# Kernel tuning notes

Measured on AMD Instinct MI355X. Metric: run time of the kernel, lower is better.

The kernel has to match this reference:

```python
import jax, jax.numpy as jnp
import numpy as np

# dims: batch, nodes, d_node, d_edge, d_attn_hid, heads, d_node_hid, d_edge_hid, layers
B, N, DN, DE, DH, H, DNH, DEH, L = 2, 256, 128, 64, 128, 8, 512, 256, 2
DHH = DH // H  # per-head dim
SCALE = 1.0 / (DH ** 0.5)  # source scales by full d_hid, not per-head dim


def _ln(x, g, b):
    m = jnp.mean(x, -1, keepdims=True)
    v = jnp.mean((x - m) ** 2, -1, keepdims=True)
    return (x - m) * jax.lax.rsqrt(v + 1e-5) * g + b


def _gelu(x):
    return jax.nn.gelu(x, approximate=False)  # torch nn.GELU default = exact erf


def setup_inputs() -> dict:
    key = jax.random.key(0)
    ks = iter(jax.random.split(key, 40))
    def w(shape, scale=0.02):
        return jax.random.normal(next(ks), shape, jnp.float32) * scale
    return {
        "node_features": jax.random.normal(next(ks), (B, N, DN), jnp.float32),
        "edge_features": jax.random.normal(next(ks), (B, N, N, DE), jnp.float32),
        "Wqkv_n": w((L, DN, 3 * DH)),
        "Wqkv_e": w((L, DE, 4 * DH)),
        "Wo": w((L, DH, DN)), "bo": jnp.zeros((L, DN), jnp.float32),
        "Wl0": w((L, DN, DN)), "bl0": jnp.zeros((L, DN), jnp.float32),
        "ln0_g": jnp.ones((L, DN), jnp.float32), "ln0_b": jnp.zeros((L, DN), jnp.float32),
        "Wm1": w((L, DN, DNH)), "Wm2": w((L, DNH, DN)), "bm2": jnp.zeros((L, DN), jnp.float32),
        "ln1_g": jnp.ones((L, DN), jnp.float32), "ln1_b": jnp.zeros((L, DN), jnp.float32),
        "We0": w((L, 2 * DE, DEH)), "be0": jnp.zeros((L, DEH), jnp.float32),
        "Ws": w((L, DN, DEH)), "bs": jnp.zeros((L, DEH), jnp.float32),
        "Wt": w((L, DN, DEH)), "bt": jnp.zeros((L, DEH), jnp.float32),
        "We1": w((L, DEH, DE)), "be1": jnp.zeros((L, DE), jnp.float32),
        "eln0_g": jnp.ones((L, DE), jnp.float32), "eln0_b": jnp.zeros((L, DE), jnp.float32),
        "Wem1": w((L, DE, DEH)), "Wem2": w((L, DEH, DE)), "bem2": jnp.zeros((L, DE), jnp.float32),
        "eln1_g": jnp.ones((L, DE), jnp.float32), "eln1_b": jnp.zeros((L, DE), jnp.float32),
    }


def _forward(node_features, edge_features, Wqkv_n, Wqkv_e, Wo, bo, Wl0, bl0,
             ln0_g, ln0_b, Wm1, Wm2, bm2, ln1_g, ln1_b, We0, be0, Ws, bs, Wt, bt,
             We1, be1, eln0_g, eln0_b, Wem1, Wem2, bem2, eln1_g, eln1_b):
    x, e = node_features, edge_features
    for l in range(L):
        # --- RTAttention (modulate_v=True, eval mode) ---
        qkv_n = (x @ Wqkv_n[l]).reshape(B, N, H, 3 * DHH).transpose(0, 2, 1, 3)  # b h n 3d
        qn, kn, vn = jnp.split(qkv_n, 3, axis=-1)
        qkv_e = (e @ Wqkv_e[l]).reshape(B, N, N, H, 4 * DHH).transpose(0, 3, 1, 2, 4)  # b h i j 4d
        eq, ek, ev, em = jnp.split(qkv_e, 4, axis=-1)
        q = qn[:, :, :, None, :] + eq            # b h i j d
        k = kn[:, :, None, :, :] + ek            # b h i j d
        v = vn[:, :, None, :, :] * em + ev       # modulated values
        dots = SCALE * jnp.einsum('bhijd,bhijd->bhij', q, k)
        attn = jax.nn.softmax(dots, axis=-1)
        out = jnp.einsum('bhij,bhijd->bhid', attn, v)
        out = out.transpose(0, 2, 1, 3).reshape(B, N, DH)
        attn_out = out @ Wo[l] + bo[l]
        # --- node updates: ln(x + lin0(attn)); ln(x + mlp(x)) ---
        x = _ln(x + (attn_out @ Wl0[l] + bl0[l]), ln0_g[l], ln0_b[l])
        x = _ln(x + (_gelu(x @ Wm1[l]) @ Wm2[l] + bm2[l]), ln1_g[l], ln1_b[l])
        # --- edge updates (EdgeLayer) ---
        src = (x @ Ws[l] + bs[l])[:, :, None, :]   # broadcast over target j
        tgt = (x @ Wt[l] + bt[l])[:, None, :, :]   # broadcast over source i
        ecat = jnp.concatenate([e, e.transpose(0, 2, 1, 3)], axis=-1)  # [e_ij, e_ji]
        h = _gelu(ecat @ We0[l] + be0[l] + src + tgt)
        e = _ln(e + (h @ We1[l] + be1[l]), eln0_g[l], eln0_b[l])
        e = _ln(e + (_gelu(e @ Wem1[l]) @ Wem2[l] + bem2[l]), eln1_g[l], eln1_b[l])
    return x, e


def reference(node_features, edge_features, Wqkv_n, Wqkv_e, Wo, bo, Wl0, bl0,
              ln0_g, ln0_b, Wm1, Wm2, bm2, ln1_g, ln1_b, We0, be0, Ws, bs, Wt, bt,
              We1, be1, eln0_g, eln0_b, Wem1, Wem2, bem2, eln1_g, eln1_b):
    return _forward(node_features, edge_features, Wqkv_n, Wqkv_e, Wo, bo, Wl0, bl0,
                    ln0_g, ln0_b, Wm1, Wm2, bm2, ln1_g, ln1_b, We0, be0, Ws, bs, Wt, bt,
                    We1, be1, eln0_g, eln0_b, Wem1, Wem2, bem2, eln1_g, eln1_b)
```

## Files before the change

### kernel.cpp

```cpp
#include <hip/hip_runtime.h>
#include <hip/hip_bf16.h>
#include <stdint.h>

#define BB 2
#define NN 256
#define DN 128
#define DE 64
#define DH 128
#define NH 8
#define DHH 16
#define DNH 512
#define DEH 256
#define NL 2
#define SCALE_ATT 0.08838834764831845f

typedef __hip_bfloat16 bf16;
typedef __attribute__((ext_vector_type(8))) short short8;
typedef __attribute__((ext_vector_type(4))) float f32x4;

__device__ __forceinline__ float gelu_f(float x) {
  return 0.5f * x * (1.0f + erff(x * 0.70710678118654752f));
}
__device__ __forceinline__ float gelu_t(float x) {
  float m2u = x * fmaf(x * x, -0.07135481627f, -1.59576912161f);
  float e = __expf(m2u);
  return x * __builtin_amdgcn_rcpf(1.f + e);
}

__device__ __forceinline__ float wave_sum(float v) {
#pragma unroll
  for (int o = 32; o > 0; o >>= 1) v += __shfl_xor(v, o, 64);
  return v;
}

__device__ __forceinline__ short f2bf(float f) {
  union { float f; uint32_t u; } v{f};
  uint32_t r = (v.u + 0x7FFFu + ((v.u >> 16) & 1u)) >> 16;
  return (short)r;
}
__device__ __forceinline__ float bf2f(short s) {
  union { uint32_t u; float f; } v;
  v.u = ((uint32_t)(uint16_t)s) << 16;
  return v.f;
}

__global__ void k_detect(const uint32_t* g8, const uint32_t* g13, int* flag) {
  if (threadIdx.x == 0 && blockIdx.x == 0) {
    uint32_t a = g8[0], b = g13[0];
    *flag = (a == 0x3F803F80u || b == 0x3F803F80u) ? 1 : 0;
  }
}

struct CastArgs {
  const void* src[30];
  float* dst[30];
  int n[30];
  const int* flag;
};

__global__ __launch_bounds__(256) void k_cast_all(CastArgs a) {
  int ti = blockIdx.y;
  float* d = a.dst[ti];
  int n = a.n[ti];
  int stride = gridDim.x * blockDim.x;
  if (*a.flag) {
    const bf16* s = (const bf16*)a.src[ti];
    for (int i = blockIdx.x * blockDim.x + threadIdx.x; i < n; i += stride)
      d[i] = __bfloat162float(s[i]);
  } else {
    const float* s = (const float*)a.src[ti];
    for (int i = blockIdx.x * blockDim.x + threadIdx.x; i < n; i += stride)
      d[i] = s[i];
  }
}

__global__ __launch_bounds__(256) void k_cast_e(const void* __restrict__ src,
                                                short* __restrict__ dst,
                                                const int* __restrict__ flag) {
  const int n8 = BB * NN * NN * DE / 8;
  int stride = gridDim.x * blockDim.x;
  if (*flag) {
    const uint4* s = (const uint4*)src;
    uint4* d = (uint4*)dst;
    for (int i = blockIdx.x * blockDim.x + threadIdx.x; i < n8; i += stride) d[i] = s[i];
  } else {
    const float4* s = (const float4*)src;
    for (int i = blockIdx.x * blockDim.x + threadIdx.x; i < n8; i += stride) {
      float4 a = s[2 * i], b = s[2 * i + 1];
      short* o = dst + 8 * i;
      o[0] = f2bf(a.x); o[1] = f2bf(a.y); o[2] = f2bf(a.z); o[3] = f2bf(a.w);
      o[4] = f2bf(b.x); o[5] = f2bf(b.y); o[6] = f2bf(b.z); o[7] = f2bf(b.w);
    }
  }
}

__global__ __launch_bounds__(256) void k_cast_out(const float* __restrict__ x,
                                                  const short* __restrict__ e,
                                                  void* __restrict__ out_v,
                                                  const int* __restrict__ flag) {
  const int nx = BB * NN * DN;
  const int total = nx + BB * NN * NN * DE;
  int stride = gridDim.x * blockDim.x;
  if (*flag) {
    short* out = (short*)out_v;
    for (int i = blockIdx.x * blockDim.x + threadIdx.x; i < total; i += stride)
      out[i] = (i < nx) ? f2bf(x[i]) : e[i - nx];
  } else {
    float* out = (float*)out_v;
    for (int i = blockIdx.x * blockDim.x + threadIdx.x; i < total; i += stride)
      out[i] = (i < nx) ? x[i] : bf2f(e[i - nx]);
  }
}

struct WtJob { const float* src; short* dst; int K; int N; };
struct WtArgs { WtJob job[10]; };
__global__ __launch_bounds__(256) void k_wtrans_all(WtArgs a) {
  WtJob j = a.job[blockIdx.y];
  int total = j.K * j.N;
  int stride = gridDim.x * 256;
  for (int idx = blockIdx.x * 256 + threadIdx.x; idx < total; idx += stride) {
    int k = idx / j.N, n = idx - k * j.N;
    j.dst[n * j.K + k] = f2bf(j.src[idx]);
  }
}

__global__ __launch_bounds__(128) void k_node_qkv(const float* __restrict__ x,
                                                  const float* __restrict__ W,
                                                  float* __restrict__ qkv) {
  int row = blockIdx.x;
  __shared__ float xs[DN];
  int t = threadIdx.x;
  xs[t] = x[row * DN + t];
  __syncthreads();
#pragma unroll
  for (int c0 = 0; c0 < 384; c0 += 128) {
    int c = c0 + t;
    float a = 0.f;
    for (int k = 0; k < DN; ++k) a = fmaf(xs[k], W[k * 384 + c], a);
    qkv[row * 384 + c] = a;
  }
}

__global__ __launch_bounds__(256) void k_attn_fused(
    const short* __restrict__ e, const short* __restrict__ WqeT,
    const float* __restrict__ qkv, float* __restrict__ o_buf) {
  int i = blockIdx.x, b = blockIdx.y;
  __shared__ short est[256 * 72];
  __shared__ float sp[NH * NN];
  __shared__ float qnl[DH];
  int t = threadIdx.x;
  for (int idx = t; idx < 2048; idx += 256) {
    int j = idx >> 3, c8 = (idx & 7) * 8;
    *(short8*)(est + j * 72 + c8) =
        *(const short8*)(e + ((size_t)(b * NN + i) * NN + j) * DE + c8);
  }
  if (t < DH) qnl[t] = qkv[(size_t)(b * NN + i) * 384 + (t >> 4) * 48 + (t & 15)];
  __syncthreads();

  int wv = t >> 6, lane = t & 63, g8 = lane >> 4, lo = lane & 15;

  {
    short8 bq[2][2][2];
#pragma unroll
    for (int hh = 0; hh < 2; ++hh)
#pragma unroll
      for (int p = 0; p < 2; ++p)
#pragma unroll
        for (int ks = 0; ks < 2; ++ks)
          bq[hh][p][ks] = *(const short8*)(
              WqeT + (size_t)(((wv * 2 + hh) * 4 + p) * 16 + lo) * 64 + ks * 32 + g8 * 8);
    for (int mt = 0; mt < 16; ++mt) {
      short8 a0 = *(const short8*)(est + (mt * 16 + lo) * 72 + g8 * 8);
      short8 a1 = *(const short8*)(est + (mt * 16 + lo) * 72 + 32 + g8 * 8);
#pragma unroll
      for (int hh = 0; hh < 2; ++hh) {
        int h = wv * 2 + hh;
        float kn4[4];
#pragma unroll
        for (int r = 0; r < 4; ++r)
          kn4[r] = qkv[(size_t)(b * NN + mt * 16 + g8 * 4 + r) * 384 + h * 48 + 16 + lo];
        f32x4 cq = {0.f, 0.f, 0.f, 0.f}, ck = {0.f, 0.f, 0.f, 0.f};
        cq = __builtin_amdgcn_mfma_f32_16x16x32_bf16(a0, bq[hh][0][0], cq, 0, 0, 0);
        cq = __builtin_amdgcn_mfma_f32_16x16x32_bf16(a1, bq[hh][0][1], cq, 0, 0, 0);
        ck = __builtin_amdgcn_mfma_f32_16x16x32_bf16(a0, bq[hh][1][0], ck, 0, 0, 0);
        ck = __builtin_amdgcn_mfma_f32_16x16x32_bf16(a1, bq[hh][1][1], ck, 0, 0, 0);
        float qv = qnl[h * 16 + lo];
#pragma unroll
        for (int r = 0; r < 4; ++r) {
          int j = mt * 16 + g8 * 4 + r;
          float s = (qv + cq[r]) * (kn4[r] + ck[r]);
#pragma unroll
          for (int off = 1; off < 16; off <<= 1) s += __shfl_xor(s, off, 64);
          if (lo == 0) sp[h * NN + j] = s * SCALE_ATT;
        }
      }
    }
  }
  __syncthreads();

#pragma unroll
  for (int hh = 0; hh < 2; ++hh) {
    int h = wv * 2 + hh;
    float v[4];
#pragma unroll
    for (int q = 0; q < 4; ++q) v[q] = sp[h * NN + lane + 64 * q];
    float m = fmaxf(fmaxf(v[0], v[1]), fmaxf(v[2], v[3]));
#pragma unroll
    for (int o = 32; o > 0; o >>= 1) m = fmaxf(m, __shfl_xor(m, o, 64));
    float l = 0.f;
#pragma unroll
    for (int q = 0; q < 4; ++q) { v[q] = __expf(v[q] - m); l += v[q]; }
    l = wave_sum(l);
    float inv = 1.f / l;
#pragma unroll
    for (int q = 0; q < 4; ++q) sp[h * NN + lane + 64 * q] = v[q] * inv;
  }
  __syncthreads();

  {
    short8 bv[2][2][2];
#pragma unroll
    for (int hh = 0; hh < 2; ++hh)
#pragma unroll
      for (int p = 0; p < 2; ++p)
#pragma unroll
        for (int ks = 0; ks < 2; ++ks)
          bv[hh][p][ks] = *(const short8*)(
              WqeT + (size_t)(((wv * 2 + hh) * 4 + 2 + p) * 16 + lo) * 64 + ks * 32 + g8 * 8);
    float oacc[2] = {0.f, 0.f};
    for (int mt = 0; mt < 16; ++mt) {
      short8 a0 = *(const short8*)(est + (mt * 16 + lo) * 72 + g8 * 8);
      short8 a1 = *(const short8*)(est + (mt * 16 + lo) * 72 + 32 + g8 * 8);
#pragma unroll
      for (int hh = 0; hh < 2; ++hh) {
        int h = wv * 2 + hh;
        float vn4[4];
#pragma unroll
        for (int r = 0; r < 4; ++r)
          vn4[r] = qkv[(size_t)(b * NN + mt * 16 + g8 * 4 + r) * 384 + h * 48 + 32 + lo];
        f32x4 cv = {0.f, 0.f, 0.f, 0.f}, cm = {0.f, 0.f, 0.f, 0.f};
        cv = __builtin_amdgcn_mfma_f32_16x16x32_bf16(a0, bv[hh][0][0], cv, 0, 0, 0);
        cv = __builtin_amdgcn_mfma_f32_16x16x32_bf16(a1, bv[hh][0][1], cv, 0, 0, 0);
        cm = __builtin_amdgcn_mfma_f32_16x16x32_bf16(a0, bv[hh][1][0], cm, 0, 0, 0);
        cm = __builtin_amdgcn_mfma_f32_16x16x32_bf16(a1, bv[hh][1][1], cm, 0, 0, 0);
#pragma unroll
        for (int r = 0; r < 4; ++r) {
          int j = mt * 16 + g8 * 4 + r;
          float vv = fmaf(vn4[r], cm[r], cv[r]);
          oacc[hh] = fmaf(sp[h * NN + j], vv, oacc[hh]);
        }
      }
    }
#pragma unroll
    for (int hh = 0; hh < 2; ++hh) {
      int h = wv * 2 + hh;
      float o = oacc[hh];
      o += __shfl_xor(o, 16, 64);
      o += __shfl_xor(o, 32, 64);
      if (g8 == 0) o_buf[(size_t)(b * NN + i) * DH + h * 16 + lo] = o;
    }
  }
}

__global__ __launch_bounds__(128) void k_node_fused(
    const float* __restrict__ o_buf,
    const float* __restrict__ Wo, const float* __restrict__ bo,
    const float* __restrict__ Wl0, const float* __restrict__ bl0,
    const float* __restrict__ g0, const float* __restrict__ b0n,
    const float* __restrict__ Wm1, const float* __restrict__ Wm2,
    const float* __restrict__ bm2, const float* __restrict__ g1,
    const float* __restrict__ b1n, const float* __restrict__ Ws,
    const float* __restrict__ bs, const float* __restrict__ Wt,
    const float* __restrict__ bt, const float* __restrict__ WqnN,
    float* __restrict__ qkv, float* __restrict__ srcb,
    float* __restrict__ tgtb, float* __restrict__ x) {
  int i = blockIdx.x, b = blockIdx.y;
  int row = b * NN + i;
  __shared__ float orow[DH];
  __shared__ float t1[DH];
  __shared__ float xs[DN];
  __shared__ float hs[DNH];
  __shared__ float red[4];
  int t = threadIdx.x;
  orow[t] = o_buf[(size_t)row * DH + t];
  __syncthreads();
  {
    float a = bo[t];
    for (int k = 0; k < DH; ++k) a = fmaf(orow[k], Wo[k * DN + t], a);
    t1[t] = a;
  }
  __syncthreads();
  {
    float y = bl0[t] + x[row * DN + t];
    for (int k = 0; k < DN; ++k) y = fmaf(t1[k], Wl0[k * DN + t], y);
    float s1 = wave_sum(y), s2 = wave_sum(y * y);
    if ((t & 63) == 0) { red[t >> 6] = s1; red[2 + (t >> 6)] = s2; }
    __syncthreads();
    float mean = (red[0] + red[1]) * (1.f / 128.f);
    float var = (red[2] + red[3]) * (1.f / 128.f) - mean * mean;
    float rr = rsqrtf(var + 1e-5f);
    xs[t] = (y - mean) * rr * g0[t] + b0n[t];
  }
  __syncthreads();
#pragma unroll
  for (int p = 0; p < 4; ++p) {
    int c = t + 128 * p;
    float a = 0.f;
    for (int k = 0; k < DN; ++k) a = fmaf(xs[k], Wm1[k * DNH + c], a);
    hs[c] = gelu_f(a);
  }
  __syncthreads();
  {
    float y = bm2[t] + xs[t];
    for (int k = 0; k < DNH; ++k) y = fmaf(hs[k], Wm2[k * DN + t], y);
    float s1 = wave_sum(y), s2 = wave_sum(y * y);
    if ((t & 63) == 0) { red[t >> 6] = s1; red[2 + (t >> 6)] = s2; }
    __syncthreads();
    float mean = (red[0] + red[1]) * (1.f / 128.f);
    float var = (red[2] + red[3]) * (1.f / 128.f) - mean * mean;
    float rr = rsqrtf(var + 1e-5f);
    float x2 = (y - mean) * rr * g1[t] + b1n[t];
    x[row * DN + t] = x2;
    xs[t] = x2;
  }
  __syncthreads();
#pragma unroll
  for (int half = 0; half < 2; ++half) {
    int c = t + 128 * half;
    float a = bs[c], cc = bt[c];
    for (int k = 0; k < DN; ++k) {
      float xv = xs[k];
      a = fmaf(xv, Ws[k * DEH + c], a);
      cc = fmaf(xv, Wt[k * DEH + c], cc);
    }
    srcb[(size_t)row * DEH + c] = a;
    tgtb[(size_t)row * DEH + c] = cc;
  }
  if (WqnN) {
#pragma unroll
    for (int p = 0; p < 3; ++p) {
      int c = t + 128 * p;
      float a = 0.f;
      for (int k = 0; k < DN; ++k) a = fmaf(xs[k], WqnN[k * 384 + c], a);
      qkv[(size_t)row * 384 + c] = a;
    }
  }
}

__global__ __launch_bounds__(256) void k_edge_fused(
    const short* __restrict__ e_in, const short* __restrict__ W0T,
    const float* __restrict__ b0, const short* __restrict__ W1T,
    const float* __restrict__ b1, const float* __restrict__ srcb,
    const float* __restrict__ tgtb, const float* __restrict__ g,
    const float* __restrict__ bb, const short* __restrict__ Wm1T,
    const short* __restrict__ Wm2T, const float* __restrict__ bm2,
    const float* __restrict__ gm, const float* __restrict__ bbm,
    short* __restrict__ e_out) {
  int jt = blockIdx.x, i = blockIdx.y, b = blockIdx.z;
  int j0 = jt * 64;
  __shared__ short hidT[64 * 264];
  int t = threadIdx.x;
  int wv = t >> 6, lane = t & 63, g8 = lane >> 4, lo = lane & 15;
  int nq = wv * 64;
  int m0 = wv * 16;

  {
    float bias_n[4];
#pragma unroll
    for (int nt = 0; nt < 4; ++nt)
      bias_n[nt] = b0[nq + nt * 16 + lo] + srcb[(size_t)(b * NN + i) * DEH + nq + nt * 16 + lo];
    short8 bfr1[4][4];
#pragma unroll
    for (int nt = 0; nt < 4; ++nt)
#pragma unroll
      for (int ks = 0; ks < 4; ++ks)
        bfr1[nt][ks] =
            *(const short8*)(W0T + (size_t)(nq + nt * 16 + lo) * 128 + ks * 32 + g8 * 8);
#pragma unroll
    for (int mt = 0; mt < 4; ++mt) {
      int mrow = mt * 16 + lo;
      float tg[4][4];
#pragma unroll
      for (int nt = 0; nt < 4; ++nt)
#pragma unroll
        for (int r = 0; r < 4; ++r)
          tg[nt][r] = tgtb[((size_t)(b * NN) + j0 + mt * 16 + g8 * 4 + r) * DEH +
                           nq + nt * 16 + lo];
      short8 a[4];
      const short* eA = e_in + ((size_t)(b * NN + i) * NN + j0 + mrow) * DE;
#pragma unroll
      for (int ks = 0; ks < 2; ++ks) a[ks] = *(const short8*)(eA + ks * 32 + g8 * 8);
      const short* eT = e_in + ((size_t)(b * NN + j0 + mrow) * NN + i) * DE;
#pragma unroll
      for (int ks = 0; ks < 2; ++ks) a[2 + ks] = *(const short8*)(eT + ks * 32 + g8 * 8);
      f32x4 acc[4];
#pragma unroll
      for (int nt = 0; nt < 4; ++nt) {
        f32x4 c = {0.f, 0.f, 0.f, 0.f};
#pragma unroll
        for (int ks = 0; ks < 4; ++ks)
          c = __builtin_amdgcn_mfma_f32_16x16x32_bf16(a[ks], bfr1[nt][ks], c, 0, 0, 0);
        acc[nt] = c;
      }
#pragma unroll
      for (int nt = 0; nt < 4; ++nt) {
        int n = nq + nt * 16 + lo;
#pragma unroll
        for (int r = 0; r < 4; ++r) {
          int m = mt * 16 + g8 * 4 + r;
          hidT[m * 264 + n] = f2bf(gelu_t(acc[nt][r] + bias_n[nt] + tg[nt][r]));
        }
      }
    }
  }
  __syncthreads();

  float emid[4][4];
  {
    float resv[4][4];
#pragma unroll
    for (int nt = 0; nt < 4; ++nt)
#pragma unroll
      for (int r = 0; r < 4; ++r)
        resv[nt][r] = bf2f(e_in[((size_t)(b * NN + i) * NN + j0 + m0 + g8 * 4 + r) * DE +
                                nt * 16 + lo]);
    short8 a2[8];
#pragma unroll
    for (int ks = 0; ks < 8; ++ks)
      a2[ks] = *(const short8*)(hidT + (m0 + lo) * 264 + ks * 32 + g8 * 8);
    f32x4 acc2[4];
#pragma unroll
    for (int nt = 0; nt < 4; ++nt) {
      f32x4 c = {0.f, 0.f, 0.f, 0.f};
      const short* bp = W1T + (size_t)(nt * 16 + lo) * 256;
#pragma unroll
      for (int ks = 0; ks < 8; ++ks)
        c = __builtin_amdgcn_mfma_f32_16x16x32_bf16(
            a2[ks], *(const short8*)(bp + ks * 32 + g8 * 8), c, 0, 0, 0);
      acc2[nt] = c;
    }
#pragma unroll
    for (int nt = 0; nt < 4; ++nt) {
      int n = nt * 16 + lo;
      float bb1 = b1[n];
#pragma unroll
      for (int r = 0; r < 4; ++r) emid[nt][r] = acc2[nt][r] + bb1 + resv[nt][r];
    }
#pragma unroll
    for (int r = 0; r < 4; ++r) {
      float s = emid[0][r] + emid[1][r] + emid[2][r] + emid[3][r];
      float q = emid[0][r] * emid[0][r] + emid[1][r] * emid[1][r] +
                emid[2][r] * emid[2][r] + emid[3][r] * emid[3][r];
#pragma unroll
      for (int off = 1; off < 16; off <<= 1) {
        s += __shfl_xor(s, off, 64);
        q += __shfl_xor(q, off, 64);
      }
      float mean = s * (1.f / 64.f);
      float var = q * (1.f / 64.f) - mean * mean;
      float rr = rsqrtf(var + 1e-5f);
      int m = m0 + g8 * 4 + r;
#pragma unroll
      for (int nt = 0; nt < 4; ++nt) {
        int n = nt * 16 + lo;
        float v = (emid[nt][r] - mean) * rr * g[n] + bb[n];
        emid[nt][r] = v;
        hidT[m * 264 + n] = f2bf(v);
      }
    }
  }

  {
    short8 a3[2];
#pragma unroll
    for (int ks = 0; ks < 2; ++ks)
      a3[ks] = *(const short8*)(hidT + (m0 + lo) * 264 + ks * 32 + g8 * 8);
    for (int nt = 0; nt < 16; ++nt) {
      f32x4 c = {0.f, 0.f, 0.f, 0.f};
      const short* bp = Wm1T + (size_t)(nt * 16 + lo) * 64;
#pragma unroll
      for (int ks = 0; ks < 2; ++ks)
        c = __builtin_amdgcn_mfma_f32_16x16x32_bf16(
            a3[ks], *(const short8*)(bp + ks * 32 + g8 * 8), c, 0, 0, 0);
      int n = nt * 16 + lo;
#pragma unroll
      for (int r = 0; r < 4; ++r)
        hidT[(m0 + g8 * 4 + r) * 264 + n] = f2bf(gelu_t(c[r]));
    }
  }

  {
    short8 a4[8];
#pragma unroll
    for (int ks = 0; ks < 8; ++ks)
      a4[ks] = *(const short8*)(hidT + (m0 + lo) * 264 + ks * 32 + g8 * 8);
    f32x4 acc4[4];
#pragma unroll
    for (int nt = 0; nt < 4; ++nt) {
      f32x4 c = {0.f, 0.f, 0.f, 0.f};
      const short* bp = Wm2T + (size_t)(nt * 16 + lo) * 256;
#pragma unroll
      for (int ks = 0; ks < 8; ++ks)
        c = __builtin_amdgcn_mfma_f32_16x16x32_bf16(
            a4[ks], *(const short8*)(bp + ks * 32 + g8 * 8), c, 0, 0, 0);
      acc4[nt] = c;
    }
    float vals[4][4];
#pragma unroll
    for (int nt = 0; nt < 4; ++nt) {
      int n = nt * 16 + lo;
      float bv = bm2[n];
#pragma unroll
      for (int r = 0; r < 4; ++r) vals[nt][r] = acc4[nt][r] + bv + emid[nt][r];
    }
#pragma unroll
    for (int r = 0; r < 4; ++r) {
      float s = vals[0][r] + vals[1][r] + vals[2][r] + vals[3][r];
      float q = vals[0][r] * vals[0][r] + vals[1][r] * vals[1][r] +
                vals[2][r] * vals[2][r] + vals[3][r] * vals[3][r];
#pragma unroll
      for (int off = 1; off < 16; off <<= 1) {
        s += __shfl_xor(s, off, 64);
        q += __shfl_xor(q, off, 64);
      }
      float mean = s * (1.f / 64.f);
      float var = q * (1.f / 64.f) - mean * mean;
      float rr = rsqrtf(var + 1e-5f);
      int m = m0 + g8 * 4 + r;
#pragma unroll
      for (int nt = 0; nt < 4; ++nt) {
        int n = nt * 16 + lo;
        e_out[((size_t)(b * NN + i) * NN + j0 + m) * DE + n] =
            f2bf((vals[nt][r] - mean) * rr * gm[n] + bbm[n]);
      }
    }
  }
}

extern "C" void kernel_launch(void* const* d_in, const int* in_sizes, int n_in,
                              void* d_out, int out_size, void* d_ws, size_t ws_size,
                              hipStream_t stream) {
  float* ws = (float*)d_ws;
  int* flag = (int*)ws;
  size_t off = 64;
  auto alloc = [&](size_t n) {
    float* p = ws + off;
    off += (n + 63) & ~(size_t)63;
    return p;
  };
  float* x_f = alloc((size_t)BB * NN * DN);
  short* e_a = (short*)alloc((size_t)BB * NN * NN * DE / 2);
  short* e_b = (short*)alloc((size_t)BB * NN * NN * DE / 2);
  float* qkv = alloc((size_t)BB * NN * 384);
  float* o_buf = alloc((size_t)BB * NN * DH);
  float* srcb = alloc((size_t)BB * NN * DEH);
  float* tgtb = alloc((size_t)BB * NN * DEH);
  short* WqeT = (short*)alloc(NL * 512 * 64 / 2);
  short* We0T = (short*)alloc(NL * 256 * 128 / 2);
  short* We1T = (short*)alloc(NL * 64 * 256 / 2);
  short* Wem1T = (short*)alloc(NL * 256 * 64 / 2);
  short* Wem2T = (short*)alloc(NL * 64 * 256 / 2);

  float* wf[30];
  wf[0] = x_f;
  wf[1] = x_f;
  CastArgs ca;
  int ntens = n_in < 30 ? n_in : 30;
  for (int idx = 0; idx < ntens; ++idx) {
    if (idx >= 2) wf[idx] = alloc((size_t)in_sizes[idx]);
    ca.src[idx] = d_in[idx];
    ca.dst[idx] = wf[idx];
    ca.n[idx] = (idx == 1) ? 0 : in_sizes[idx];
  }
  ca.flag = flag;

  k_detect<<<1, 64, 0, stream>>>((const uint32_t*)d_in[8], (const uint32_t*)d_in[13], flag);
  k_cast_all<<<dim3(64, ntens), dim3(256), 0, stream>>>(ca);
  k_cast_e<<<1024, 256, 0, stream>>>(d_in[1], e_a, flag);
  WtArgs wa;
  for (int l = 0; l < NL; ++l) {
    wa.job[l * 5 + 0] = {wf[3] + (size_t)l * DE * 512, WqeT + (size_t)l * 512 * 64, DE, 512};
    wa.job[l * 5 + 1] = {wf[15] + (size_t)l * 128 * 256, We0T + (size_t)l * 256 * 128, 128, 256};
    wa.job[l * 5 + 2] = {wf[21] + (size_t)l * 256 * 64, We1T + (size_t)l * 64 * 256, 256, 64};
    wa.job[l * 5 + 3] = {wf[25] + (size_t)l * 64 * 256, Wem1T + (size_t)l * 256 * 64, 64, 256};
    wa.job[l * 5 + 4] = {wf[26] + (size_t)l * 256 * 64, Wem2T + (size_t)l * 64 * 256, 256, 64};
  }
  k_wtrans_all<<<dim3(64, 10), 256, 0, stream>>>(wa);

  k_node_qkv<<<BB * NN, 128, 0, stream>>>(x_f, wf[2], qkv);

  for (int l = 0; l < NL; ++l) {
    const float* Wo = wf[4] + (size_t)l * DH * DN;
    const float* bo = wf[5] + (size_t)l * DN;
    const float* Wl0 = wf[6] + (size_t)l * DN * DN;
    const float* bl0 = wf[7] + (size_t)l * DN;
    const float* g0 = wf[8] + (size_t)l * DN;
    const float* b0n = wf[9] + (size_t)l * DN;
    const float* Wm1 = wf[10] + (size_t)l * DN * DNH;
    const float* Wm2 = wf[11] + (size_t)l * DNH * DN;
    const float* bm2 = wf[12] + (size_t)l * DN;
    const float* g1 = wf[13] + (size_t)l * DN;
    const float* b1n = wf[14] + (size_t)l * DN;
    const float* be0 = wf[16] + (size_t)l * DEH;
    const float* Wsw = wf[17] + (size_t)l * DN * DEH;
    const float* bsw = wf[18] + (size_t)l * DEH;
    const float* Wtw = wf[19] + (size_t)l * DN * DEH;
    const float* btw = wf[20] + (size_t)l * DEH;
    const float* be1 = wf[22] + (size_t)l * DE;
    const float* eg0 = wf[23] + (size_t)l * DE;
    const float* eb0 = wf[24] + (size_t)l * DE;
    const float* bem2 = wf[27] + (size_t)l * DE;
    const float* eg1 = wf[28] + (size_t)l * DE;
    const float* eb1 = wf[29] + (size_t)l * DE;
    const float* WqnNext = (l + 1 < NL) ? (wf[2] + (size_t)(l + 1) * DN * 3 * DH) : nullptr;

    const short* e_cur = (l == 0) ? e_a : e_b;
    short* e_nxt = (l == 0) ? e_b : e_a;

    k_attn_fused<<<dim3(NN, BB), 256, 0, stream>>>(
        e_cur, WqeT + (size_t)l * 512 * 64, qkv, o_buf);
    k_node_fused<<<dim3(NN, BB), 128, 0, stream>>>(
        o_buf, Wo, bo, Wl0, bl0, g0, b0n, Wm1, Wm2, bm2, g1, b1n,
        Wsw, bsw, Wtw, btw, WqnNext, qkv, srcb, tgtb, x_f);
    k_edge_fused<<<dim3(NN / 64, NN, BB), 256, 0, stream>>>(
        e_cur, We0T + (size_t)l * 256 * 128, be0, We1T + (size_t)l * 64 * 256, be1,
        srcb, tgtb, eg0, eb0,
        Wem1T + (size_t)l * 256 * 64, Wem2T + (size_t)l * 64 * 256, bem2, eg1, eb1,
        e_nxt);
  }
  k_cast_out<<<1024, 256, 0, stream>>>(x_f, e_a, d_out, flag);
}
```

Before: 625.6 us.

## Split attention over head groups, drop LDS staging, swizzle edge hidden LDS

The attention kernel now launches one block per (row, head-group of 4, batch), with each wave owning a single head. It reads edge tiles straight from global memory instead of staging them in LDS, and it drops the block-wide barriers. This doubles the grid and shrinks LDS use to raise occupancy, at the cost of each edge row being read twice from global/L2. The edge kernel replaces the padded LDS layout (stride 264) with an XOR swizzle (stride 256) to cut LDS footprint while avoiding bank conflicts, and adds occupancy hints to both kernels' launch bounds.

```diff
diff --git a/kernel.cpp b/kernel.cpp
--- a/kernel.cpp
+++ b/kernel.cpp
@@ -42,6 +42,10 @@
   union { uint32_t u; float f; } v;
   v.u = ((uint32_t)(uint16_t)s) << 16;
   return v.f;
+}
+
+__device__ __forceinline__ int hswz(int m, int n) {
+  return m * 256 + (n ^ ((m & 7) << 3));
 }
 
 __global__ void k_detect(const uint32_t* g8, const uint32_t* g13, int* flag) {
@@ -141,69 +145,56 @@
   }
 }
 
-__global__ __launch_bounds__(256) void k_attn_fused(
+__global__ __launch_bounds__(256, 4) void k_attn_fused(
     const short* __restrict__ e, const short* __restrict__ WqeT,
     const float* __restrict__ qkv, float* __restrict__ o_buf) {
-  int i = blockIdx.x, b = blockIdx.y;
-  __shared__ short est[256 * 72];
-  __shared__ float sp[NH * NN];
-  __shared__ float qnl[DH];
+  int i = blockIdx.x, hs = blockIdx.y, b = blockIdx.z;
+  __shared__ float sp[4 * NN];
   int t = threadIdx.x;
-  for (int idx = t; idx < 2048; idx += 256) {
-    int j = idx >> 3, c8 = (idx & 7) * 8;
-    *(short8*)(est + j * 72 + c8) =
-        *(const short8*)(e + ((size_t)(b * NN + i) * NN + j) * DE + c8);
-  }
-  if (t < DH) qnl[t] = qkv[(size_t)(b * NN + i) * 384 + (t >> 4) * 48 + (t & 15)];
-  __syncthreads();
-
   int wv = t >> 6, lane = t & 63, g8 = lane >> 4, lo = lane & 15;
-
-  {
-    short8 bq[2][2][2];
-#pragma unroll
-    for (int hh = 0; hh < 2; ++hh)
-#pragma unroll
-      for (int p = 0; p < 2; ++p)
-#pragma unroll
-        for (int ks = 0; ks < 2; ++ks)
-          bq[hh][p][ks] = *(const short8*)(
-              WqeT + (size_t)(((wv * 2 + hh) * 4 + p) * 16 + lo) * 64 + ks * 32 + g8 * 8);
+  int h = hs * 4 + wv;
+  const short* erow = e + (size_t)(b * NN + i) * NN * DE;
+  size_t qbase = (size_t)(b * NN) * 384;
+
+  float qv = qkv[(size_t)(b * NN + i) * 384 + h * 48 + lo];
+
+  {
+    short8 bq[2][2];
+#pragma unroll
+    for (int p = 0; p < 2; ++p)
+#pragma unroll
+      for (int ks = 0; ks < 2; ++ks)
+        bq[p][ks] = *(const short8*)(
+            WqeT + (size_t)((h * 4 + p) * 16 + lo) * 64 + ks * 32 + g8 * 8);
+#pragma unroll 2
     for (int mt = 0; mt < 16; ++mt) {
-      short8 a0 = *(const short8*)(est + (mt * 16 + lo) * 72 + g8 * 8);
-      short8 a1 = *(const short8*)(est + (mt * 16 + lo) * 72 + 32 + g8 * 8);
-#pragma unroll
-      for (int hh = 0; hh < 2; ++hh) {
-        int h = wv * 2 + hh;
-        float kn4[4];
-#pragma unroll
-        for (int r = 0; r < 4; ++r)
-          kn4[r] = qkv[(size_t)(b * NN + mt * 16 + g8 * 4 + r) * 384 + h * 48 + 16 + lo];
-        f32x4 cq = {0.f, 0.f, 0.f, 0.f}, ck = {0.f, 0.f, 0.f, 0.f};
-        cq = __builtin_amdgcn_mfma_f32_16x16x32_bf16(a0, bq[hh][0][0], cq, 0, 0, 0);
-        cq = __builtin_amdgcn_mfma_f32_16x16x32_bf16(a1, bq[hh][0][1], cq, 0, 0, 0);
-        ck = __builtin_amdgcn_mfma_f32_16x16x32_bf16(a0, bq[hh][1][0], ck, 0, 0, 0);
-        ck = __builtin_amdgcn_mfma_f32_16x16x32_bf16(a1, bq[hh][1][1], ck, 0, 0, 0);
-        float qv = qnl[h * 16 + lo];
-#pragma unroll
-        for (int r = 0; r < 4; ++r) {
-          int j = mt * 16 + g8 * 4 + r;
-          float s = (qv + cq[r]) * (kn4[r] + ck[r]);
-#pragma unroll
-          for (int off = 1; off < 16; off <<= 1) s += __shfl_xor(s, off, 64);
-          if (lo == 0) sp[h * NN + j] = s * SCALE_ATT;
-        }
-      }
-    }
-  }
-  __syncthreads();
-
-#pragma unroll
-  for (int hh = 0; hh < 2; ++hh) {
-    int h = wv * 2 + hh;
+      const short* ea = erow + (mt * 16 + lo) * DE;
+      short8 a0 = *(const short8*)(ea + g8 * 8);
+      short8 a1 = *(const short8*)(ea + 32 + g8 * 8);
+      float kn4[4];
+#pragma unroll
+      for (int r = 0; r < 4; ++r)
+        kn4[r] = qkv[qbase + (size_t)(mt * 16 + g8 * 4 + r) * 384 + h * 48 + 16 + lo];
+      f32x4 cq = {0.f, 0.f, 0.f, 0.f}, ck = {0.f, 0.f, 0.f, 0.f};
+      cq = __builtin_amdgcn_mfma_f32_16x16x32_bf16(a0, bq[0][0], cq, 0, 0, 0);
+      cq = __builtin_amdgcn_mfma_f32_16x16x32_bf16(a1, bq[0][1], cq, 0, 0, 0);
+      ck = __builtin_amdgcn_mfma_f32_16x16x32_bf16(a0, bq[1][0], ck, 0, 0, 0);
+      ck = __builtin_amdgcn_mfma_f32_16x16x32_bf16(a1, bq[1][1], ck, 0, 0, 0);
+#pragma unroll
+      for (int r = 0; r < 4; ++r) {
+        int j = mt * 16 + g8 * 4 + r;
+        float s = (qv + cq[r]) * (kn4[r] + ck[r]);
+#pragma unroll
+        for (int off = 1; off < 16; off <<= 1) s += __shfl_xor(s, off, 64);
+        if (lo == 0) sp[wv * NN + j] = s * SCALE_ATT;
+      }
+    }
+  }
+
+  {
     float v[4];
 #pragma unroll
-    for (int q = 0; q < 4; ++q) v[q] = sp[h * NN + lane + 64 * q];
+    for (int q = 0; q < 4; ++q) v[q] = sp[wv * NN + lane + 64 * q];
     float m = fmaxf(fmaxf(v[0], v[1]), fmaxf(v[2], v[3]));
 #pragma unroll
     for (int o = 32; o > 0; o >>= 1) m = fmaxf(m, __shfl_xor(m, o, 64));
@@ -213,52 +204,42 @@
     l = wave_sum(l);
     float inv = 1.f / l;
 #pragma unroll
-    for (int q = 0; q < 4; ++q) sp[h * NN + lane + 64 * q] = v[q] * inv;
-  }
-  __syncthreads();
-
-  {
-    short8 bv[2][2][2];
-#pragma unroll
-    for (int hh = 0; hh < 2; ++hh)
-#pragma unroll
-      for (int p = 0; p < 2; ++p)
-#pragma unroll
-        for (int ks = 0; ks < 2; ++ks)
-          bv[hh][p][ks] = *(const short8*)(
-              WqeT + (size_t)(((wv * 2 + hh) * 4 + 2 + p) * 16 + lo) * 64 + ks * 32 + g8 * 8);
-    float oacc[2] = {0.f, 0.f};
+    for (int q = 0; q < 4; ++q) sp[wv * NN + lane + 64 * q] = v[q] * inv;
+  }
+
+  {
+    short8 bv[2][2];
+#pragma unroll
+    for (int p = 0; p < 2; ++p)
+#pragma unroll
+      for (int ks = 0; ks < 2; ++ks)
+        bv[p][ks] = *(const short8*)(
+            WqeT + (size_t)((h * 4 + 2 + p) * 16 + lo) * 64 + ks * 32 + g8 * 8);
+    float oacc = 0.f;
+#pragma unroll 2
     for (int mt = 0; mt < 16; ++mt) {
-      short8 a0 = *(const short8*)(est + (mt * 16 + lo) * 72 + g8 * 8);
-      short8 a1 = *(const short8*)(est + (mt * 16 + lo) * 72 + 32 + g8 * 8);
-#pragma unroll
-      for (int hh = 0; hh < 2; ++hh) {
-        int h = wv * 2 + hh;
-        float vn4[4];
-#pragma unroll
-        for (int r = 0; r < 4; ++r)
-          vn4[r] = qkv[(size_t)(b * NN + mt * 16 + g8 * 4 + r) * 384 + h * 48 + 32 + lo];
-        f32x4 cv = {0.f, 0.f, 0.f, 0.f}, cm = {0.f, 0.f, 0.f, 0.f};
-        cv = __builtin_amdgcn_mfma_f32_16x16x32_bf16(a0, bv[hh][0][0], cv, 0, 0, 0);
-        cv = __builtin_amdgcn_mfma_f32_16x16x32_bf16(a1, bv[hh][0][1], cv, 0, 0, 0);
-        cm = __builtin_amdgcn_mfma_f32_16x16x32_bf16(a0, bv[hh][1][0], cm, 0, 0, 0);
-        cm = __builtin_amdgcn_mfma_f32_16x16x32_bf16(a1, bv[hh][1][1], cm, 0, 0, 0);
-#pragma unroll
-        for (int r = 0; r < 4; ++r) {
-          int j = mt * 16 + g8 * 4 + r;
-          float vv = fmaf(vn4[r], cm[r], cv[r]);
-          oacc[hh] = fmaf(sp[h * NN + j], vv, oacc[hh]);
-        }
-      }
-    }
-#pragma unroll
-    for (int hh = 0; hh < 2; ++hh) {
-      int h = wv * 2 + hh;
-      float o = oacc[hh];
-      o += __shfl_xor(o, 16, 64);
-      o += __shfl_xor(o, 32, 64);
-      if (g8 == 0) o_buf[(size_t)(b * NN + i) * DH + h * 16 + lo] = o;
-    }
+      const short* ea = erow + (mt * 16 + lo) * DE;
+      short8 a0 = *(const short8*)(ea + g8 * 8);
+      short8 a1 = *(const short8*)(ea + 32 + g8 * 8);
+      float vn4[4];
+#pragma unroll
+      for (int r = 0; r < 4; ++r)
+        vn4[r] = qkv[qbase + (size_t)(mt * 16 + g8 * 4 + r) * 384 + h * 48 + 32 + lo];
+      f32x4 cv = {0.f, 0.f, 0.f, 0.f}, cm = {0.f, 0.f, 0.f, 0.f};
+      cv = __builtin_amdgcn_mfma_f32_16x16x32_bf16(a0, bv[0][0], cv, 0, 0, 0);
+      cv = __builtin_amdgcn_mfma_f32_16x16x32_bf16(a1, bv[0][1], cv, 0, 0, 0);
+      cm = __builtin_amdgcn_mfma_f32_16x16x32_bf16(a0, bv[1][0], cm, 0, 0, 0);
+      cm = __builtin_amdgcn_mfma_f32_16x16x32_bf16(a1, bv[1][1], cm, 0, 0, 0);
+#pragma unroll
+      for (int r = 0; r < 4; ++r) {
+        int j = mt * 16 + g8 * 4 + r;
+        float vv = fmaf(vn4[r], cm[r], cv[r]);
+        oacc = fmaf(sp[wv * NN + j], vv, oacc);
+      }
+    }
+    oacc += __shfl_xor(oacc, 16, 64);
+    oacc += __shfl_xor(oacc, 32, 64);
+    if (g8 == 0) o_buf[(size_t)(b * NN + i) * DH + h * 16 + lo] = oacc;
   }
 }
 
@@ -347,7 +328,7 @@
   }
 }
 
-__global__ __launch_bounds__(256) void k_edge_fused(
+__global__ __launch_bounds__(256, 5) void k_edge_fused(
     const short* __restrict__ e_in, const short* __restrict__ W0T,
     const float* __restrict__ b0, const short* __restrict__ W1T,
     const float* __restrict__ b1, const float* __restrict__ srcb,
@@ -358,7 +339,7 @@
     short* __restrict__ e_out) {
   int jt = blockIdx.x, i = blockIdx.y, b = blockIdx.z;
   int j0 = jt * 64;
-  __shared__ short hidT[64 * 264];
+  __shared__ short hidT[64 * 256];
   int t = threadIdx.x;
   int wv = t >> 6, lane = t & 63, g8 = lane >> 4, lo = lane & 15;
   int nq = wv * 64;
@@ -408,7 +389,7 @@
 #pragma unroll
         for (int r = 0; r < 4; ++r) {
           int m = mt * 16 + g8 * 4 + r;
-          hidT[m * 264 + n] = f2bf(gelu_t(acc[nt][r] + bias_n[nt] + tg[nt][r]));
+          hidT[hswz(m, n)] = f2bf(gelu_t(acc[nt][r] + bias_n[nt] + tg[nt][r]));
         }
       }
     }
@@ -427,7 +408,7 @@
     short8 a2[8];
 #pragma unroll
     for (int ks = 0; ks < 8; ++ks)
-      a2[ks] = *(const short8*)(hidT + (m0 + lo) * 264 + ks * 32 + g8 * 8);
+      a2[ks] = *(const short8*)(hidT + hswz(m0 + lo, ks * 32 + g8 * 8));
     f32x4 acc2[4];
 #pragma unroll
     for (int nt = 0; nt < 4; ++nt) {
@@ -465,7 +446,7 @@
         int n = nt * 16 + lo;
         float v = (emid[nt][r] - mean) * rr * g[n] + bb[n];
         emid[nt][r] = v;
-        hidT[m * 264 + n] = f2bf(v);
+        hidT[hswz(m, n)] = f2bf(v);
       }
     }
   }
@@ -474,7 +455,8 @@
     short8 a3[2];
 #pragma unroll
     for (int ks = 0; ks < 2; ++ks)
-      a3[ks] = *(const short8*)(hidT + (m0 + lo) * 264 + ks * 32 + g8 * 8);
+      a3[ks] = *(const short8*)(hidT + hswz(m0 + lo, ks * 32 + g8 * 8));
+#pragma unroll 4
     for (int nt = 0; nt < 16; ++nt) {
       f32x4 c = {0.f, 0.f, 0.f, 0.f};
       const short* bp = Wm1T + (size_t)(nt * 16 + lo) * 64;
@@ -485,7 +467,7 @@
       int n = nt * 16 + lo;
 #pragma unroll
       for (int r = 0; r < 4; ++r)
-        hidT[(m0 + g8 * 4 + r) * 264 + n] = f2bf(gelu_t(c[r]));
+        hidT[hswz(m0 + g8 * 4 + r, n)] = f2bf(gelu_t(c[r]));
     }
   }
 
@@ -493,7 +475,7 @@
     short8 a4[8];
 #pragma unroll
     for (int ks = 0; ks < 8; ++ks)
-      a4[ks] = *(const short8*)(hidT + (m0 + lo) * 264 + ks * 32 + g8 * 8);
+      a4[ks] = *(const short8*)(hidT + hswz(m0 + lo, ks * 32 + g8 * 8));
     f32x4 acc4[4];
 #pragma unroll
     for (int nt = 0; nt < 4; ++nt) {
@@ -617,7 +599,7 @@
     const short* e_cur = (l == 0) ? e_a : e_b;
     short* e_nxt = (l == 0) ? e_b : e_a;
 
-    k_attn_fused<<<dim3(NN, BB), 256, 0, stream>>>(
+    k_attn_fused<<<dim3(NN, 2, BB), 256, 0, stream>>>(
         e_cur, WqeT + (size_t)l * 512 * 64, qkv, o_buf);
     k_node_fused<<<dim3(NN, BB), 128, 0, stream>>>(
         o_buf, Wo, bo, Wl0, bl0, g0, b0n, Wm1, Wm2, bm2, g1, b1n,
```

Measured after the change: 695.9 us. +11.2%, slower.

## Split node-kernel matvecs across 256 threads and hoist residual loads in edge kernel

Applied to the files above, without the earlier changes.

The per-row node kernel now runs 256 threads instead of 128. Each matvec over K is split into two halves, and the partial sums are reduced through shared memory, which shortens the serial FMA chains. In the edge kernel the residual edge loads move ahead of the barrier so their latency overlaps the sync, and one loop gets a partial unroll hint. The Wem2 offset expression is rewritten, but 256*64 equals 64*256, so the value is unchanged. The cost is extra barriers and shared-memory traffic for the partial sums.

```diff
diff --git a/kernel.cpp b/kernel.cpp
--- a/kernel.cpp
+++ b/kernel.cpp
@@ -262,7 +262,7 @@
   }
 }
 
-__global__ __launch_bounds__(128) void k_node_fused(
+__global__ __launch_bounds__(256) void k_node_fused(
     const float* __restrict__ o_buf,
     const float* __restrict__ Wo, const float* __restrict__ bo,
     const float* __restrict__ Wl0, const float* __restrict__ bl0,
@@ -277,25 +277,40 @@
   int i = blockIdx.x, b = blockIdx.y;
   int row = b * NN + i;
   __shared__ float orow[DH];
-  __shared__ float t1[DH];
+  __shared__ float t1s[DH];
   __shared__ float xs[DN];
-  __shared__ float hs[DNH];
+  __shared__ float hsb[DNH];
+  __shared__ float part[256];
   __shared__ float red[4];
   int t = threadIdx.x;
-  orow[t] = o_buf[(size_t)row * DH + t];
-  __syncthreads();
-  {
-    float a = bo[t];
-    for (int k = 0; k < DH; ++k) a = fmaf(orow[k], Wo[k * DN + t], a);
-    t1[t] = a;
-  }
-  __syncthreads();
-  {
-    float y = bl0[t] + x[row * DN + t];
-    for (int k = 0; k < DN; ++k) y = fmaf(t1[k], Wl0[k * DN + t], y);
+  int col = t & 127, kh = t >> 7;
+  if (t < DH) orow[t] = o_buf[(size_t)row * DH + t];
+  __syncthreads();
+  {
+    float a = 0.f;
+    int k0 = kh * 64;
+    for (int k = k0; k < k0 + 64; ++k) a = fmaf(orow[k], Wo[k * DN + col], a);
+    part[t] = a;
+  }
+  __syncthreads();
+  if (t < DH) t1s[t] = part[t] + part[t + 128] + bo[t];
+  __syncthreads();
+  {
+    float a = 0.f;
+    int k0 = kh * 64;
+    for (int k = k0; k < k0 + 64; ++k) a = fmaf(t1s[k], Wl0[k * DN + col], a);
+    part[t] = a;
+  }
+  __syncthreads();
+  if (t < DN) {
+    float y = part[t] + part[t + 128] + bl0[t] + x[(size_t)row * DN + t];
     float s1 = wave_sum(y), s2 = wave_sum(y * y);
     if ((t & 63) == 0) { red[t >> 6] = s1; red[2 + (t >> 6)] = s2; }
-    __syncthreads();
+    part[t] = y;
+  }
+  __syncthreads();
+  if (t < DN) {
+    float y = part[t];
     float mean = (red[0] + red[1]) * (1.f / 128.f);
     float var = (red[2] + red[3]) * (1.f / 128.f) - mean * mean;
     float rr = rsqrtf(var + 1e-5f);
@@ -303,46 +318,56 @@
   }
   __syncthreads();
 #pragma unroll
-  for (int p = 0; p < 4; ++p) {
-    int c = t + 128 * p;
+  for (int p = 0; p < 2; ++p) {
+    int c = t + 256 * p;
     float a = 0.f;
     for (int k = 0; k < DN; ++k) a = fmaf(xs[k], Wm1[k * DNH + c], a);
-    hs[c] = gelu_f(a);
-  }
-  __syncthreads();
-  {
-    float y = bm2[t] + xs[t];
-    for (int k = 0; k < DNH; ++k) y = fmaf(hs[k], Wm2[k * DN + t], y);
+    hsb[c] = gelu_f(a);
+  }
+  __syncthreads();
+  {
+    float a = 0.f;
+    int k0 = kh * 256;
+    for (int k = k0; k < k0 + 256; ++k) a = fmaf(hsb[k], Wm2[k * DN + col], a);
+    part[t] = a;
+  }
+  __syncthreads();
+  if (t < DN) {
+    float y = part[t] + part[t + 128] + bm2[t] + xs[t];
     float s1 = wave_sum(y), s2 = wave_sum(y * y);
     if ((t & 63) == 0) { red[t >> 6] = s1; red[2 + (t >> 6)] = s2; }
-    __syncthreads();
+    part[t] = y;
+  }
+  __syncthreads();
+  if (t < DN) {
+    float y = part[t];
     float mean = (red[0] + red[1]) * (1.f / 128.f);
     float var = (red[2] + red[3]) * (1.f / 128.f) - mean * mean;
     float rr = rsqrtf(var + 1e-5f);
     float x2 = (y - mean) * rr * g1[t] + b1n[t];
-    x[row * DN + t] = x2;
+    x[(size_t)row * DN + t] = x2;
     xs[t] = x2;
   }
   __syncthreads();
-#pragma unroll
-  for (int half = 0; half < 2; ++half) {
-    int c = t + 128 * half;
-    float a = bs[c], cc = bt[c];
+  {
+    float a = bs[t], cc = bt[t];
     for (int k = 0; k < DN; ++k) {
       float xv = xs[k];
-      a = fmaf(xv, Ws[k * DEH + c], a);
-      cc = fmaf(xv, Wt[k * DEH + c], cc);
-    }
-    srcb[(size_t)row * DEH + c] = a;
-    tgtb[(size_t)row * DEH + c] = cc;
+      a = fmaf(xv, Ws[k * DEH + t], a);
+      cc = fmaf(xv, Wt[k * DEH + t], cc);
+    }
+    srcb[(size_t)row * DEH + t] = a;
+    tgtb[(size_t)row * DEH + t] = cc;
   }
   if (WqnN) {
 #pragma unroll
-    for (int p = 0; p < 3; ++p) {
-      int c = t + 128 * p;
-      float a = 0.f;
-      for (int k = 0; k < DN; ++k) a = fmaf(xs[k], WqnN[k * 384 + c], a);
-      qkv[(size_t)row * 384 + c] = a;
+    for (int p = 0; p < 2; ++p) {
+      int c = t + 256 * p;
+      if (c < 384) {
+        float a = 0.f;
+        for (int k = 0; k < DN; ++k) a = fmaf(xs[k], WqnN[k * 384 + c], a);
+        qkv[(size_t)row * 384 + c] = a;
+      }
     }
   }
 }
@@ -413,17 +438,17 @@
       }
     }
   }
+  float resv[4][4];
+#pragma unroll
+  for (int nt = 0; nt < 4; ++nt)
+#pragma unroll
+    for (int r = 0; r < 4; ++r)
+      resv[nt][r] = bf2f(e_in[((size_t)(b * NN + i) * NN + j0 + m0 + g8 * 4 + r) * DE +
+                              nt * 16 + lo]);
   __syncthreads();
 
   float emid[4][4];
   {
-    float resv[4][4];
-#pragma unroll
-    for (int nt = 0; nt < 4; ++nt)
-#pragma unroll
-      for (int r = 0; r < 4; ++r)
-        resv[nt][r] = bf2f(e_in[((size_t)(b * NN + i) * NN + j0 + m0 + g8 * 4 + r) * DE +
-                                nt * 16 + lo]);
     short8 a2[8];
 #pragma unroll
     for (int ks = 0; ks < 8; ++ks)
@@ -475,6 +500,7 @@
 #pragma unroll
     for (int ks = 0; ks < 2; ++ks)
       a3[ks] = *(const short8*)(hidT + (m0 + lo) * 264 + ks * 32 + g8 * 8);
+#pragma unroll 4
     for (int nt = 0; nt < 16; ++nt) {
       f32x4 c = {0.f, 0.f, 0.f, 0.f};
       const short* bp = Wm1T + (size_t)(nt * 16 + lo) * 64;
@@ -583,7 +609,7 @@
     wa.job[l * 5 + 1] = {wf[15] + (size_t)l * 128 * 256, We0T + (size_t)l * 256 * 128, 128, 256};
     wa.job[l * 5 + 2] = {wf[21] + (size_t)l * 256 * 64, We1T + (size_t)l * 64 * 256, 256, 64};
     wa.job[l * 5 + 3] = {wf[25] + (size_t)l * 64 * 256, Wem1T + (size_t)l * 256 * 64, 64, 256};
-    wa.job[l * 5 + 4] = {wf[26] + (size_t)l * 256 * 64, Wem2T + (size_t)l * 64 * 256, 256, 64};
+    wa.job[l * 5 + 4] = {wf[26] + (size_t)l * 64 * 256, Wem2T + (size_t)l * 64 * 256, 256, 64};
   }
   k_wtrans_all<<<dim3(64, 10), 256, 0, stream>>>(wa);
 
@@ -619,7 +645,7 @@
 
     k_attn_fused<<<dim3(NN, BB), 256, 0, stream>>>(
         e_cur, WqeT + (size_t)l * 512 * 64, qkv, o_buf);
-    k_node_fused<<<dim3(NN, BB), 128, 0, stream>>>(
+    k_node_fused<<<dim3(NN, BB), 256, 0, stream>>>(
         o_buf, Wo, bo, Wl0, bl0, g0, b0n, Wm1, Wm2, bm2, g1, b1n,
         Wsw, bsw, Wtw, btw, WqnNext, qkv, srcb, tgtb, x_f);
     k_edge_fused<<<dim3(NN / 64, NN, BB), 256, 0, stream>>>(
```

Result: faster. 578.6 us (-7.5%).
